# Performance work log

Hardware: AMD Instinct MI355X
Metric: run time of the kernel (lower is better)

## Reference

```python
import jax, jax.numpy as jnp
import numpy as np

B, D, H, G = 32768, 768, 256, 8
GS = D // G          # group size = 96
MIN_G, MAX_G = 2, 6  # min/max active groups


def setup_inputs() -> dict:
    key = jax.random.key(0)
    ks = jax.random.split(key, 12)
    s = 0.02
    return {
        "query_embedding": jax.random.normal(ks[0], (B, D), jnp.float32),
        # router_net: Linear(D,H) -> LayerNorm(H) -> GELU -> Linear(H,H//2) -> GELU -> Linear(H//2,G)
        "w1": jax.random.normal(ks[1], (D, H), jnp.float32) * s,
        "b1": jnp.zeros((H,), jnp.float32),
        "ln_g": jnp.ones((H,), jnp.float32),
        "ln_b": jnp.zeros((H,), jnp.float32),
        "w2": jax.random.normal(ks[2], (H, H // 2), jnp.float32) * s,
        "b2": jnp.zeros((H // 2,), jnp.float32),
        "w3": jax.random.normal(ks[3], (H // 2, G), jnp.float32) * s,
        "b3": jnp.zeros((G,), jnp.float32),
        # dim_importance: Linear(D,H) -> GELU -> Linear(H,D) (bias init 2.0) -> Sigmoid
        "dw1": jax.random.normal(ks[4], (D, H), jnp.float32) * s,
        "db1": jnp.zeros((H,), jnp.float32),
        "dw2": jax.random.normal(ks[5], (H, D), jnp.float32) * s,
        "db2": jnp.full((D,), 2.0, jnp.float32),
        "group_importance": jax.random.normal(ks[6], (G,), jnp.float32) * s,
    }


def _gelu(x):
    return jax.nn.gelu(x, approximate=False)  # torch nn.GELU default = exact erf


def _layernorm(x, g, b, eps=1e-5):
    mu = jnp.mean(x, axis=-1, keepdims=True)
    var = jnp.var(x, axis=-1, keepdims=True)
    return (x - mu) * jax.lax.rsqrt(var + eps) * g + b


def reference(query_embedding, w1, b1, ln_g, ln_b, w2, b2, w3, b3,
              dw1, db1, dw2, db2, group_importance):
    x = query_embedding
    # router_net (eval mode: dropout is identity, sigmoid gating not gumbel)
    h1 = _gelu(_layernorm(x @ w1 + b1, ln_g, ln_b))
    h2 = _gelu(h1 @ w2 + b2)
    group_logits = h2 @ w3 + b3 + group_importance          # [B, G]
    group_probs = jax.nn.sigmoid(group_logits)

    # constrained hard selection: top MIN_G always on; ranks MIN_G..MAX_G-1 on iff prob > 0.5
    order = jnp.argsort(-group_probs, axis=-1)              # descending sort indices [B, G]
    sorted_probs = jnp.take_along_axis(group_probs, order, axis=-1)
    ranks = jnp.arange(G)
    act_sorted = jnp.where(ranks < MIN_G, 1.0,
                           jnp.where(ranks < MAX_G,
                                     (sorted_probs > 0.5).astype(jnp.float32), 0.0))
    b_idx = jnp.arange(x.shape[0])[:, None]
    hard_mask = jnp.zeros_like(group_probs).at[b_idx, order].set(act_sorted)
    # straight-through estimator
    group_selection = hard_mask - jax.lax.stop_gradient(group_probs) + group_probs

    # expand each group decision over its group_size dims -> [B, D]
    group_mask = jnp.repeat(group_selection, GS, axis=-1)

    dim_weights = jax.nn.sigmoid(_gelu(x @ dw1 + db1) @ dw2 + db2)  # [B, D]
    mask = group_mask * dim_weights

    active_groups = jnp.mean(jnp.sum((group_probs > 0.5).astype(jnp.float32), axis=-1))
    group_usage = jnp.mean((group_probs > 0.5).astype(jnp.float32), axis=0)
    f = jnp.mean(group_probs, axis=0)
    load_balance = G * jnp.sum(f * (1.0 / G))
    active_dims = jnp.mean(jnp.sum((mask > 0.5).astype(jnp.float32), axis=-1))

    return (mask, group_mask, dim_weights, group_probs, group_selection,
            active_groups, group_usage, load_balance, active_dims)
```

## Files before the change

kernel.cpp:

```cpp
#include <hip/hip_runtime.h>
#include <math.h>

#define NB 32768
#define ND 768
#define NH 256
#define NG 8
#define GSZ 96

typedef __attribute__((ext_vector_type(8))) short short8_t;
typedef __attribute__((ext_vector_type(4))) float f32x4;

__device__ __forceinline__ float gelu_exact(float v) {
    return 0.5f * v * (1.0f + erff(v * 0.7071067811865475f));
}
__device__ __forceinline__ float sigmoidf_(float v) {
    return 1.0f / (1.0f + expf(-v));
}
__device__ __forceinline__ unsigned short f2bf(float f) {
    union { float f; unsigned u; } a; a.f = f;
    unsigned r = a.u + 0x7FFF + ((a.u >> 16) & 1);
    return (unsigned short)(r >> 16);
}
__device__ __forceinline__ void f2bf2(float f, unsigned short& hi, unsigned short& lo) {
    union { float f; unsigned u; } a; a.f = f;
    unsigned r = a.u + 0x7FFF + ((a.u >> 16) & 1);
    hi = (unsigned short)(r >> 16);
    union { unsigned u; float f; } hf; hf.u = (r >> 16) << 16;
    float rem = f - hf.f;
    union { float f; unsigned u; } b; b.f = rem;
    unsigned r2 = b.u + 0x7FFF + ((b.u >> 16) & 1);
    lo = (unsigned short)(r2 >> 16);
}

__global__ __launch_bounds__(256) void cvt_wall(
    const float* __restrict__ w1, const float* __restrict__ dw1,
    const float* __restrict__ dw2, const float* __restrict__ w2,
    unsigned short* __restrict__ w1Th, unsigned short* __restrict__ w1Tl,
    unsigned short* __restrict__ dw1T, unsigned short* __restrict__ dw2T,
    unsigned short* __restrict__ w2Th, unsigned short* __restrict__ w2Tl,
    float* __restrict__ scal)
{
    const int b = blockIdx.x, t = threadIdx.x;
    if (b < 96) {
        int idx = b * 256 + t;
        int k8 = idx >> 8, c = idx & 255;
        short8_t h, lo;
        #pragma unroll
        for (int j = 0; j < 8; ++j) {
            unsigned short hi_, lo_;
            f2bf2(w1[(size_t)(k8 * 8 + j) * 256 + c], hi_, lo_);
            h[j] = (short)hi_; lo[j] = (short)lo_;
        }
        *(short8_t*)(w1Th + (size_t)c * 768 + k8 * 8) = h;
        *(short8_t*)(w1Tl + (size_t)c * 768 + k8 * 8) = lo;
    } else if (b < 192) {
        int idx = (b - 96) * 256 + t;
        int k8 = idx >> 8, c = idx & 255;
        short8_t h;
        #pragma unroll
        for (int j = 0; j < 8; ++j)
            h[j] = (short)f2bf(dw1[(size_t)(k8 * 8 + j) * 256 + c]);
        *(short8_t*)(dw1T + (size_t)c * 768 + k8 * 8) = h;
    } else if (b < 288) {
        int idx = (b - 192) * 256 + t;
        int k8 = idx / 768, c = idx - k8 * 768;
        short8_t h;
        #pragma unroll
        for (int j = 0; j < 8; ++j)
            h[j] = (short)f2bf(dw2[(size_t)(k8 * 8 + j) * 768 + c]);
        *(short8_t*)(dw2T + (size_t)c * 256 + k8 * 8) = h;
    } else if (b < 304) {
        int idx = (b - 288) * 256 + t;
        int k8 = idx >> 7, c = idx & 127;
        short8_t h, lo;
        #pragma unroll
        for (int j = 0; j < 8; ++j) {
            unsigned short hi_, lo_;
            f2bf2(w2[(size_t)(k8 * 8 + j) * 128 + c], hi_, lo_);
            h[j] = (short)hi_; lo[j] = (short)lo_;
        }
        *(short8_t*)(w2Th + (size_t)c * 256 + k8 * 8) = h;
        *(short8_t*)(w2Tl + (size_t)c * 256 + k8 * 8) = lo;
    } else {
        if (t < 11) scal[t] = 0.0f;
    }
}

__global__ __launch_bounds__(256) void mfma_u1(
    const float* __restrict__ x, const unsigned short* __restrict__ BTh,
    const unsigned short* __restrict__ BTl, float* __restrict__ u1)
{
    __shared__ unsigned short Ah[128][40];
    __shared__ unsigned short Al[128][40];
    __shared__ unsigned short Bh[128][40];
    __shared__ unsigned short Bl[128][40];

    const int tid = threadIdx.x;
    const int l = tid & 63;
    const int w = tid >> 6;
    const int wm = w >> 1, wn = w & 1;
    const int lg = l >> 4, lr = l & 15;
    const int rb = blockIdx.x >> 1;
    const int cb = blockIdx.x & 1;
    const int rowsBase = rb * 128, colBase = cb * 128;

    f32x4 acc[4][4];
    #pragma unroll
    for (int mi = 0; mi < 4; ++mi)
        #pragma unroll
        for (int ni = 0; ni < 4; ++ni) acc[mi][ni] = (f32x4){0.f, 0.f, 0.f, 0.f};

    for (int kb = 0; kb < ND; kb += 32) {
        #pragma unroll
        for (int m = 0; m < 2; ++m) {
            int flat = m * 256 + tid;
            int row = flat >> 2, seg = flat & 3;
            const float* src = x + (size_t)(rowsBase + row) * ND + kb + seg * 8;
            float4 v0 = *(const float4*)src;
            float4 v1 = *(const float4*)(src + 4);
            float f[8] = {v0.x, v0.y, v0.z, v0.w, v1.x, v1.y, v1.z, v1.w};
            short8_t ph, pl;
            #pragma unroll
            for (int j = 0; j < 8; ++j) {
                unsigned short hi_, lo_;
                f2bf2(f[j], hi_, lo_);
                ph[j] = (short)hi_; pl[j] = (short)lo_;
            }
            *(short8_t*)&Ah[row][seg * 8] = ph;
            *(short8_t*)&Al[row][seg * 8] = pl;
        }
        #pragma unroll
        for (int m = 0; m < 2; ++m) {
            int flat = m * 256 + tid;
            int col = flat >> 2, seg = flat & 3;
            size_t off = (size_t)(colBase + col) * ND + kb + seg * 8;
            *(short8_t*)&Bh[col][seg * 8] = *(const short8_t*)(BTh + off);
            *(short8_t*)&Bl[col][seg * 8] = *(const short8_t*)(BTl + off);
        }
        __syncthreads();

        short8_t afh[4], afl[4], bfh[4], bfl[4];
        #pragma unroll
        for (int mi = 0; mi < 4; ++mi) {
            afh[mi] = *(const short8_t*)&Ah[wm * 64 + mi * 16 + lr][lg * 8];
            afl[mi] = *(const short8_t*)&Al[wm * 64 + mi * 16 + lr][lg * 8];
        }
        #pragma unroll
        for (int ni = 0; ni < 4; ++ni) {
            bfh[ni] = *(const short8_t*)&Bh[wn * 64 + ni * 16 + lr][lg * 8];
            bfl[ni] = *(const short8_t*)&Bl[wn * 64 + ni * 16 + lr][lg * 8];
        }
        #pragma unroll
        for (int mi = 0; mi < 4; ++mi)
            #pragma unroll
            for (int ni = 0; ni < 4; ++ni) {
                acc[mi][ni] = __builtin_amdgcn_mfma_f32_16x16x32_bf16(
                    afl[mi], bfh[ni], acc[mi][ni], 0, 0, 0);
                acc[mi][ni] = __builtin_amdgcn_mfma_f32_16x16x32_bf16(
                    afh[mi], bfl[ni], acc[mi][ni], 0, 0, 0);
                acc[mi][ni] = __builtin_amdgcn_mfma_f32_16x16x32_bf16(
                    afh[mi], bfh[ni], acc[mi][ni], 0, 0, 0);
            }
        __syncthreads();
    }

    #pragma unroll
    for (int ni = 0; ni < 4; ++ni) {
        int col = colBase + wn * 64 + ni * 16 + lr;
        #pragma unroll
        for (int mi = 0; mi < 4; ++mi) {
            int rbase = rowsBase + wm * 64 + mi * 16 + lg * 4;
            #pragma unroll
            for (int j = 0; j < 4; ++j)
                u1[(size_t)(rbase + j) * 256 + col] = acc[mi][ni][j];
        }
    }
}

__global__ __launch_bounds__(256) void k1_epi(
    const float* __restrict__ u1, const float* __restrict__ b1,
    const float* __restrict__ lng, const float* __restrict__ lnb,
    float* __restrict__ h1)
{
    const int wv = threadIdx.x >> 6, l = threadIdx.x & 63;
    const int row = blockIdx.x * 4 + wv;
    float4 a = *(const float4*)(u1 + (size_t)row * 256 + l * 4);
    float4 bb = *(const float4*)(b1 + l * 4);
    float u[4] = {a.x + bb.x, a.y + bb.y, a.z + bb.z, a.w + bb.w};
    float s = u[0] + u[1] + u[2] + u[3];
    float q = u[0]*u[0] + u[1]*u[1] + u[2]*u[2] + u[3]*u[3];
    #pragma unroll
    for (int o = 1; o < 64; o <<= 1) {
        s += __shfl_xor(s, o);
        q += __shfl_xor(q, o);
    }
    float mean = s * (1.0f / 256.0f);
    float var  = q * (1.0f / 256.0f) - mean * mean;
    float rstd = rsqrtf(var + 1e-5f);
    float4 g = *(const float4*)(lng + l * 4);
    float4 be = *(const float4*)(lnb + l * 4);
    float4 o;
    o.x = gelu_exact((u[0] - mean) * rstd * g.x + be.x);
    o.y = gelu_exact((u[1] - mean) * rstd * g.y + be.y);
    o.z = gelu_exact((u[2] - mean) * rstd * g.z + be.z);
    o.w = gelu_exact((u[3] - mean) * rstd * g.w + be.w);
    *(float4*)(h1 + (size_t)row * 256 + l * 4) = o;
}

__global__ __launch_bounds__(256) void mfma_u2(
    const float* __restrict__ h1, const unsigned short* __restrict__ BTh,
    const unsigned short* __restrict__ BTl, float* __restrict__ u2)
{
    __shared__ unsigned short Ah[128][40];
    __shared__ unsigned short Al[128][40];
    __shared__ unsigned short Bh[128][40];
    __shared__ unsigned short Bl[128][40];

    const int tid = threadIdx.x;
    const int l = tid & 63;
    const int w = tid >> 6;
    const int wm = w >> 1, wn = w & 1;
    const int lg = l >> 4, lr = l & 15;
    const int rowsBase = blockIdx.x * 128;

    f32x4 acc[4][4];
    #pragma unroll
    for (int mi = 0; mi < 4; ++mi)
        #pragma unroll
        for (int ni = 0; ni < 4; ++ni) acc[mi][ni] = (f32x4){0.f, 0.f, 0.f, 0.f};

    for (int kb = 0; kb < 256; kb += 32) {
        #pragma unroll
        for (int m = 0; m < 2; ++m) {
            int flat = m * 256 + tid;
            int row = flat >> 2, seg = flat & 3;
            const float* src = h1 + (size_t)(rowsBase + row) * 256 + kb + seg * 8;
            float4 v0 = *(const float4*)src;
            float4 v1 = *(const float4*)(src + 4);
            float f[8] = {v0.x, v0.y, v0.z, v0.w, v1.x, v1.y, v1.z, v1.w};
            short8_t ph, pl;
            #pragma unroll
            for (int j = 0; j < 8; ++j) {
                unsigned short hi_, lo_;
                f2bf2(f[j], hi_, lo_);
                ph[j] = (short)hi_; pl[j] = (short)lo_;
            }
            *(short8_t*)&Ah[row][seg * 8] = ph;
            *(short8_t*)&Al[row][seg * 8] = pl;
        }
        #pragma unroll
        for (int m = 0; m < 2; ++m) {
            int flat = m * 256 + tid;
            int col = flat >> 2, seg = flat & 3;
            size_t off = (size_t)col * 256 + kb + seg * 8;
            *(short8_t*)&Bh[col][seg * 8] = *(const short8_t*)(BTh + off);
            *(short8_t*)&Bl[col][seg * 8] = *(const short8_t*)(BTl + off);
        }
        __syncthreads();

        short8_t afh[4], afl[4], bfh[4], bfl[4];
        #pragma unroll
        for (int mi = 0; mi < 4; ++mi) {
            afh[mi] = *(const short8_t*)&Ah[wm * 64 + mi * 16 + lr][lg * 8];
            afl[mi] = *(const short8_t*)&Al[wm * 64 + mi * 16 + lr][lg * 8];
        }
        #pragma unroll
        for (int ni = 0; ni < 4; ++ni) {
            bfh[ni] = *(const short8_t*)&Bh[wn * 64 + ni * 16 + lr][lg * 8];
            bfl[ni] = *(const short8_t*)&Bl[wn * 64 + ni * 16 + lr][lg * 8];
        }
        #pragma unroll
        for (int mi = 0; mi < 4; ++mi)
            #pragma unroll
            for (int ni = 0; ni < 4; ++ni) {
                acc[mi][ni] = __builtin_amdgcn_mfma_f32_16x16x32_bf16(
                    afl[mi], bfh[ni], acc[mi][ni], 0, 0, 0);
                acc[mi][ni] = __builtin_amdgcn_mfma_f32_16x16x32_bf16(
                    afh[mi], bfl[ni], acc[mi][ni], 0, 0, 0);
                acc[mi][ni] = __builtin_amdgcn_mfma_f32_16x16x32_bf16(
                    afh[mi], bfh[ni], acc[mi][ni], 0, 0, 0);
            }
        __syncthreads();
    }

    #pragma unroll
    for (int ni = 0; ni < 4; ++ni) {
        int col = wn * 64 + ni * 16 + lr;
        #pragma unroll
        for (int mi = 0; mi < 4; ++mi) {
            int rbase = rowsBase + wm * 64 + mi * 16 + lg * 4;
            #pragma unroll
            for (int j = 0; j < 4; ++j)
                u2[(size_t)(rbase + j) * 128 + col] = acc[mi][ni][j];
        }
    }
}

template<int ACT, int AF32>
__global__ __launch_bounds__(256) void mfma_hi(
    const void* __restrict__ Ap, const unsigned short* __restrict__ BT,
    const float* __restrict__ bias, void* __restrict__ outp,
    int N, int K, int colBlocks)
{
    __shared__ unsigned short As[128][40];
    __shared__ unsigned short Bs[128][40];

    const int tid = threadIdx.x;
    const int l = tid & 63;
    const int w = tid >> 6;
    const int wm = w >> 1, wn = w & 1;
    const int lg = l >> 4, lr = l & 15;
    const int rb = blockIdx.x / colBlocks;
    const int cb = blockIdx.x - rb * colBlocks;
    const int rowsBase = rb * 128, colBase = cb * 128;

    f32x4 acc[4][4];
    #pragma unroll
    for (int mi = 0; mi < 4; ++mi)
        #pragma unroll
        for (int ni = 0; ni < 4; ++ni) acc[mi][ni] = (f32x4){0.f, 0.f, 0.f, 0.f};

    for (int kb = 0; kb < K; kb += 32) {
        if (AF32) {
            const float* A = (const float*)Ap;
            #pragma unroll
            for (int m = 0; m < 2; ++m) {
                int flat = m * 256 + tid;
                int row = flat >> 2, seg = flat & 3;
                const float* src = A + (size_t)(rowsBase + row) * K + kb + seg * 8;
                float4 v0 = *(const float4*)src;
                float4 v1 = *(const float4*)(src + 4);
                float f[8] = {v0.x, v0.y, v0.z, v0.w, v1.x, v1.y, v1.z, v1.w};
                short8_t h;
                #pragma unroll
                for (int j = 0; j < 8; ++j) h[j] = (short)f2bf(f[j]);
                *(short8_t*)&As[row][seg * 8] = h;
            }
        } else {
            const unsigned short* A = (const unsigned short*)Ap;
            #pragma unroll
            for (int m = 0; m < 2; ++m) {
                int flat = m * 256 + tid;
                int row = flat >> 2, seg = flat & 3;
                *(short8_t*)&As[row][seg * 8] =
                    *(const short8_t*)(A + (size_t)(rowsBase + row) * K + kb + seg * 8);
            }
        }
        #pragma unroll
        for (int m = 0; m < 2; ++m) {
            int flat = m * 256 + tid;
            int col = flat >> 2, seg = flat & 3;
            *(short8_t*)&Bs[col][seg * 8] =
                *(const short8_t*)(BT + (size_t)(colBase + col) * K + kb + seg * 8);
        }
        __syncthreads();

        short8_t af[4], bf[4];
        #pragma unroll
        for (int mi = 0; mi < 4; ++mi)
            af[mi] = *(const short8_t*)&As[wm * 64 + mi * 16 + lr][lg * 8];
        #pragma unroll
        for (int ni = 0; ni < 4; ++ni)
            bf[ni] = *(const short8_t*)&Bs[wn * 64 + ni * 16 + lr][lg * 8];
        #pragma unroll
        for (int mi = 0; mi < 4; ++mi)
            #pragma unroll
            for (int ni = 0; ni < 4; ++ni)
                acc[mi][ni] = __builtin_amdgcn_mfma_f32_16x16x32_bf16(
                    af[mi], bf[ni], acc[mi][ni], 0, 0, 0);
        __syncthreads();
    }

    #pragma unroll
    for (int ni = 0; ni < 4; ++ni) {
        int col = colBase + wn * 64 + ni * 16 + lr;
        float bv = bias[col];
        #pragma unroll
        for (int mi = 0; mi < 4; ++mi) {
            int rbase = rowsBase + wm * 64 + mi * 16 + lg * 4;
            #pragma unroll
            for (int j = 0; j < 4; ++j) {
                float v = acc[mi][ni][j] + bv;
                if (ACT == 0) {
                    ((unsigned short*)outp)[(size_t)(rbase + j) * N + col] =
                        f2bf(gelu_exact(v));
                } else {
                    ((float*)outp)[(size_t)(rbase + j) * N + col] = sigmoidf_(v);
                }
            }
        }
    }
}

__global__ __launch_bounds__(128) void k3_router(
    const float* __restrict__ u2, const float* __restrict__ w3,
    const float* __restrict__ b3, const float* __restrict__ gi,
    const float* __restrict__ b2, float* __restrict__ probsOut,
    float* __restrict__ selOut, float* __restrict__ scal)
{
    __shared__ float ws3[128][8];
    __shared__ float sAct[2], sP[2], sCnt[2][8];

    const int tid = threadIdx.x;
    *(float4*)&ws3[tid][0] = *(const float4*)(w3 + tid * 8);
    *(float4*)&ws3[tid][4] = *(const float4*)(w3 + tid * 8 + 4);
    __syncthreads();

    const int row = blockIdx.x * 128 + tid;
    const float* r0p = u2 + (size_t)row * 128;

    float accg[8];
    #pragma unroll
    for (int g = 0; g < 8; ++g) accg[g] = 0.0f;
    #pragma unroll 4
    for (int k4 = 0; k4 < 32; ++k4) {
        float4 a = *(const float4*)(r0p + k4 * 4);
        float4 bb = *(const float4*)(b2 + k4 * 4);
        float hv4[4];
        hv4[0] = gelu_exact(a.x + bb.x);
        hv4[1] = gelu_exact(a.y + bb.y);
        hv4[2] = gelu_exact(a.z + bb.z);
        hv4[3] = gelu_exact(a.w + bb.w);
        #pragma unroll
        for (int t = 0; t < 4; ++t)
            #pragma unroll
            for (int g = 0; g < 8; ++g)
                accg[g] = fmaf(hv4[t], ws3[k4 * 4 + t][g], accg[g]);
    }

    float p[8], gs[8], cnt[8];
    float actCnt = 0.0f, pSum = 0.0f;
    #pragma unroll
    for (int g = 0; g < 8; ++g) {
        float lg = accg[g] + b3[g] + gi[g];
        p[g] = sigmoidf_(lg);
    }
    #pragma unroll
    for (int g = 0; g < 8; ++g) {
        int rank = 0;
        #pragma unroll
        for (int j = 0; j < 8; ++j) {
            rank += (p[j] > p[g]) ? 1 : 0;
            rank += (j < g && p[j] == p[g]) ? 1 : 0;
        }
        float act = (rank < 2) ? 1.0f
                  : ((rank < 6) ? ((p[g] > 0.5f) ? 1.0f : 0.0f) : 0.0f);
        gs[g] = (act - p[g]) + p[g];
        float over = (p[g] > 0.5f) ? 1.0f : 0.0f;
        cnt[g] = over;
        actCnt += over;
        pSum += p[g];
    }

    *(float4*)(probsOut + (size_t)row * 8)     = *(float4*)&p[0];
    *(float4*)(probsOut + (size_t)row * 8 + 4) = *(float4*)&p[4];
    *(float4*)(selOut   + (size_t)row * 8)     = *(float4*)&gs[0];
    *(float4*)(selOut   + (size_t)row * 8 + 4) = *(float4*)&gs[4];

    #pragma unroll
    for (int o = 32; o > 0; o >>= 1) {
        actCnt += __shfl_down(actCnt, o);
        pSum   += __shfl_down(pSum, o);
        #pragma unroll
        for (int g = 0; g < 8; ++g) cnt[g] += __shfl_down(cnt[g], o);
    }
    if ((tid & 63) == 0) {
        int w = tid >> 6;
        sAct[w] = actCnt; sP[w] = pSum;
        #pragma unroll
        for (int g = 0; g < 8; ++g) sCnt[w][g] = cnt[g];
    }
    __syncthreads();
    if (tid == 0) {
        const float invB = 1.0f / 32768.0f;
        atomicAdd(&scal[0], (sAct[0] + sAct[1]) * invB);
        atomicAdd(&scal[9], (sP[0] + sP[1]) * invB);
        #pragma unroll
        for (int g = 0; g < 8; ++g)
            atomicAdd(&scal[1 + g], (sCnt[0][g] + sCnt[1][g]) * invB);
    }
}

__global__ __launch_bounds__(256) void k4_mask(
    const float* __restrict__ sel, const float* __restrict__ dwts,
    float* __restrict__ gmaskOut, float* __restrict__ maskOut,
    float* __restrict__ activeDims)
{
    const int stride = gridDim.x * 256;
    float cntF = 0.0f;
    for (int i4 = blockIdx.x * 256 + threadIdx.x; i4 < 6291456; i4 += stride) {
        int row = i4 / 192;
        int rem = i4 - row * 192;
        int g = rem / 24;
        float v = sel[(size_t)row * 8 + g];
        float4 d = *(const float4*)(dwts + (size_t)i4 * 4);
        float4 gm = {v, v, v, v};
        float4 m = {v * d.x, v * d.y, v * d.z, v * d.w};
        *(float4*)(gmaskOut + (size_t)i4 * 4) = gm;
        *(float4*)(maskOut  + (size_t)i4 * 4) = m;
        cntF += (m.x > 0.5f ? 1.0f : 0.0f) + (m.y > 0.5f ? 1.0f : 0.0f)
              + (m.z > 0.5f ? 1.0f : 0.0f) + (m.w > 0.5f ? 1.0f : 0.0f);
    }
    #pragma unroll
    for (int o = 32; o > 0; o >>= 1) cntF += __shfl_down(cntF, o);
    __shared__ float sc[4];
    if ((threadIdx.x & 63) == 0) sc[threadIdx.x >> 6] = cntF;
    __syncthreads();
    if (threadIdx.x == 0)
        atomicAdd(activeDims, (sc[0] + sc[1] + sc[2] + sc[3]) * (1.0f / 32768.0f));
}

extern "C" void kernel_launch(void* const* d_in, const int* in_sizes, int n_in,
                              void* d_out, int out_size, void* d_ws, size_t ws_size,
                              hipStream_t stream)
{
    const float* x   = (const float*)d_in[0];
    const float* w1  = (const float*)d_in[1];
    const float* b1  = (const float*)d_in[2];
    const float* lng = (const float*)d_in[3];
    const float* lnb = (const float*)d_in[4];
    const float* w2  = (const float*)d_in[5];
    const float* b2  = (const float*)d_in[6];
    const float* w3  = (const float*)d_in[7];
    const float* b3  = (const float*)d_in[8];
    const float* dw1 = (const float*)d_in[9];
    const float* db1 = (const float*)d_in[10];
    const float* dw2 = (const float*)d_in[11];
    const float* db2 = (const float*)d_in[12];
    const float* gi  = (const float*)d_in[13];

    float* out   = (float*)d_out;
    float* mask  = out;
    float* gmask = out + 25165824;
    float* dwts  = out + 50331648;
    float* probs = out + 75497472;
    float* sel   = out + 75759616;
    float* scal  = out + 76021760;

    float* u1 = mask;
    float* h1 = mask + 8388608;
    float* u2 = mask + 16777216;
    unsigned short* g1h  = (unsigned short*)gmask;
    unsigned short* w1Th = (unsigned short*)(gmask + 4194304);
    unsigned short* w1Tl = (unsigned short*)(gmask + 4292608);
    unsigned short* dw1T = (unsigned short*)(gmask + 4390912);
    unsigned short* dw2T = (unsigned short*)(gmask + 4489216);
    unsigned short* w2Th = (unsigned short*)(gmask + 4587520);
    unsigned short* w2Tl = (unsigned short*)(gmask + 4603904);

    cvt_wall<<<dim3(305), dim3(256), 0, stream>>>(
        w1, dw1, dw2, w2, w1Th, w1Tl, dw1T, dw2T, w2Th, w2Tl, scal);
    mfma_u1<<<dim3(512), dim3(256), 0, stream>>>(x, w1Th, w1Tl, u1);
    k1_epi<<<dim3(8192), dim3(256), 0, stream>>>(u1, b1, lng, lnb, h1);
    mfma_u2<<<dim3(256), dim3(256), 0, stream>>>(h1, w2Th, w2Tl, u2);
    k3_router<<<dim3(256), dim3(128), 0, stream>>>(
        u2, w3, b3, gi, b2, probs, sel, scal);
    mfma_hi<0, 1><<<dim3(512), dim3(256), 0, stream>>>(
        (const void*)x, dw1T, db1, (void*)g1h, 256, 768, 2);
    mfma_hi<1, 0><<<dim3(1536), dim3(256), 0, stream>>>(
        (const void*)g1h, dw2T, db2, (void*)dwts, 768, 256, 6);
    k4_mask<<<dim3(2048), dim3(256), 0, stream>>>(sel, dwts, gmask, mask, &scal[10]);
}
```

Measured before the change: 284.0 us.

## Fuse dim-importance GEMMs with router GEMM launch and mask epilogue

Merges the router first-layer split-bf16 GEMM and the dim_importance first-layer GEMM into one 512-thread kernel, with block role chosen by block index. Both use 128x256 tiles. The second dim_importance GEMM now computes sigmoid, the mask product and the active-dims count in its epilogue. That removes the separate pass that re-read the full dim_weights array, leaving a lighter kernel that only writes group_mask. The cost is larger tiles with more LDS per block, branches on block role, and strided scalar stores in the epilogue.

```diff
diff --git a/kernel.cpp b/kernel.cpp
--- a/kernel.cpp
+++ b/kernel.cpp
@@ -86,23 +86,24 @@
     }
 }
 
-__global__ __launch_bounds__(256) void mfma_u1(
-    const float* __restrict__ x, const unsigned short* __restrict__ BTh,
-    const unsigned short* __restrict__ BTl, float* __restrict__ u1)
+__global__ __launch_bounds__(512) void mfma_pair(
+    const float* __restrict__ x,
+    const unsigned short* __restrict__ w1Th, const unsigned short* __restrict__ w1Tl,
+    const unsigned short* __restrict__ dw1T, const float* __restrict__ db1,
+    float* __restrict__ u1, unsigned short* __restrict__ g1h)
 {
     __shared__ unsigned short Ah[128][40];
     __shared__ unsigned short Al[128][40];
-    __shared__ unsigned short Bh[128][40];
-    __shared__ unsigned short Bl[128][40];
+    __shared__ unsigned short Bh[256][40];
+    __shared__ unsigned short Bl[256][40];
 
     const int tid = threadIdx.x;
     const int l = tid & 63;
     const int w = tid >> 6;
-    const int wm = w >> 1, wn = w & 1;
+    const int wm = w >> 2, wn = w & 3;
     const int lg = l >> 4, lr = l & 15;
-    const int rb = blockIdx.x >> 1;
-    const int cb = blockIdx.x & 1;
-    const int rowsBase = rb * 128, colBase = cb * 128;
+    const bool splitRole = blockIdx.x < 256;
+    const int rowsBase = (blockIdx.x & 255) * 128;
 
     f32x4 acc[4][4];
     #pragma unroll
@@ -110,69 +111,107 @@
         #pragma unroll
         for (int ni = 0; ni < 4; ++ni) acc[mi][ni] = (f32x4){0.f, 0.f, 0.f, 0.f};
 
+    const int sArow = tid >> 2, sAseg = tid & 3;
+
     for (int kb = 0; kb < ND; kb += 32) {
-        #pragma unroll
-        for (int m = 0; m < 2; ++m) {
-            int flat = m * 256 + tid;
-            int row = flat >> 2, seg = flat & 3;
-            const float* src = x + (size_t)(rowsBase + row) * ND + kb + seg * 8;
+        {
+            const float* src = x + (size_t)(rowsBase + sArow) * ND + kb + sAseg * 8;
             float4 v0 = *(const float4*)src;
             float4 v1 = *(const float4*)(src + 4);
             float f[8] = {v0.x, v0.y, v0.z, v0.w, v1.x, v1.y, v1.z, v1.w};
-            short8_t ph, pl;
-            #pragma unroll
-            for (int j = 0; j < 8; ++j) {
-                unsigned short hi_, lo_;
-                f2bf2(f[j], hi_, lo_);
-                ph[j] = (short)hi_; pl[j] = (short)lo_;
-            }
-            *(short8_t*)&Ah[row][seg * 8] = ph;
-            *(short8_t*)&Al[row][seg * 8] = pl;
+            if (splitRole) {
+                short8_t ph, pl;
+                #pragma unroll
+                for (int j = 0; j < 8; ++j) {
+                    unsigned short hi_, lo_;
+                    f2bf2(f[j], hi_, lo_);
+                    ph[j] = (short)hi_; pl[j] = (short)lo_;
+                }
+                *(short8_t*)&Ah[sArow][sAseg * 8] = ph;
+                *(short8_t*)&Al[sArow][sAseg * 8] = pl;
+            } else {
+                short8_t ph;
+                #pragma unroll
+                for (int j = 0; j < 8; ++j) ph[j] = (short)f2bf(f[j]);
+                *(short8_t*)&Ah[sArow][sAseg * 8] = ph;
+            }
         }
         #pragma unroll
         for (int m = 0; m < 2; ++m) {
-            int flat = m * 256 + tid;
+            int flat = m * 512 + tid;
             int col = flat >> 2, seg = flat & 3;
-            size_t off = (size_t)(colBase + col) * ND + kb + seg * 8;
-            *(short8_t*)&Bh[col][seg * 8] = *(const short8_t*)(BTh + off);
-            *(short8_t*)&Bl[col][seg * 8] = *(const short8_t*)(BTl + off);
+            size_t off = (size_t)col * ND + kb + seg * 8;
+            if (splitRole) {
+                *(short8_t*)&Bh[col][seg * 8] = *(const short8_t*)(w1Th + off);
+                *(short8_t*)&Bl[col][seg * 8] = *(const short8_t*)(w1Tl + off);
+            } else {
+                *(short8_t*)&Bh[col][seg * 8] = *(const short8_t*)(dw1T + off);
+            }
         }
         __syncthreads();
 
-        short8_t afh[4], afl[4], bfh[4], bfl[4];
-        #pragma unroll
-        for (int mi = 0; mi < 4; ++mi) {
+        short8_t afh[4], bfh[4];
+        #pragma unroll
+        for (int mi = 0; mi < 4; ++mi)
             afh[mi] = *(const short8_t*)&Ah[wm * 64 + mi * 16 + lr][lg * 8];
-            afl[mi] = *(const short8_t*)&Al[wm * 64 + mi * 16 + lr][lg * 8];
-        }
+        #pragma unroll
+        for (int ni = 0; ni < 4; ++ni)
+            bfh[ni] = *(const short8_t*)&Bh[wn * 64 + ni * 16 + lr][lg * 8];
+        if (splitRole) {
+            short8_t afl[4], bfl[4];
+            #pragma unroll
+            for (int mi = 0; mi < 4; ++mi)
+                afl[mi] = *(const short8_t*)&Al[wm * 64 + mi * 16 + lr][lg * 8];
+            #pragma unroll
+            for (int ni = 0; ni < 4; ++ni)
+                bfl[ni] = *(const short8_t*)&Bl[wn * 64 + ni * 16 + lr][lg * 8];
+            #pragma unroll
+            for (int mi = 0; mi < 4; ++mi)
+                #pragma unroll
+                for (int ni = 0; ni < 4; ++ni) {
+                    acc[mi][ni] = __builtin_amdgcn_mfma_f32_16x16x32_bf16(
+                        afl[mi], bfh[ni], acc[mi][ni], 0, 0, 0);
+                    acc[mi][ni] = __builtin_amdgcn_mfma_f32_16x16x32_bf16(
+                        afh[mi], bfl[ni], acc[mi][ni], 0, 0, 0);
+                    acc[mi][ni] = __builtin_amdgcn_mfma_f32_16x16x32_bf16(
+                        afh[mi], bfh[ni], acc[mi][ni], 0, 0, 0);
+                }
+        } else {
+            #pragma unroll
+            for (int mi = 0; mi < 4; ++mi)
+                #pragma unroll
+                for (int ni = 0; ni < 4; ++ni)
+                    acc[mi][ni] = __builtin_amdgcn_mfma_f32_16x16x32_bf16(
+                        afh[mi], bfh[ni], acc[mi][ni], 0, 0, 0);
+        }
+        __syncthreads();
+    }
+
+    if (splitRole) {
         #pragma unroll
         for (int ni = 0; ni < 4; ++ni) {
-            bfh[ni] = *(const short8_t*)&Bh[wn * 64 + ni * 16 + lr][lg * 8];
-            bfl[ni] = *(const short8_t*)&Bl[wn * 64 + ni * 16 + lr][lg * 8];
-        }
-        #pragma unroll
-        for (int mi = 0; mi < 4; ++mi)
-            #pragma unroll
-            for (int ni = 0; ni < 4; ++ni) {
-                acc[mi][ni] = __builtin_amdgcn_mfma_f32_16x16x32_bf16(
-                    afl[mi], bfh[ni], acc[mi][ni], 0, 0, 0);
-                acc[mi][ni] = __builtin_amdgcn_mfma_f32_16x16x32_bf16(
-                    afh[mi], bfl[ni], acc[mi][ni], 0, 0, 0);
-                acc[mi][ni] = __builtin_amdgcn_mfma_f32_16x16x32_bf16(
-                    afh[mi], bfh[ni], acc[mi][ni], 0, 0, 0);
-            }
-        __syncthreads();
-    }
-
-    #pragma unroll
-    for (int ni = 0; ni < 4; ++ni) {
-        int col = colBase + wn * 64 + ni * 16 + lr;
-        #pragma unroll
-        for (int mi = 0; mi < 4; ++mi) {
-            int rbase = rowsBase + wm * 64 + mi * 16 + lg * 4;
-            #pragma unroll
-            for (int j = 0; j < 4; ++j)
-                u1[(size_t)(rbase + j) * 256 + col] = acc[mi][ni][j];
+            int col = wn * 64 + ni * 16 + lr;
+            #pragma unroll
+            for (int mi = 0; mi < 4; ++mi) {
+                int rbase = rowsBase + wm * 64 + mi * 16 + lg * 4;
+                #pragma unroll
+                for (int j = 0; j < 4; ++j)
+                    u1[(size_t)(rbase + j) * 256 + col] = acc[mi][ni][j];
+            }
+        }
+    } else {
+        #pragma unroll
+        for (int ni = 0; ni < 4; ++ni) {
+            int col = wn * 64 + ni * 16 + lr;
+            float bv = db1[col];
+            #pragma unroll
+            for (int mi = 0; mi < 4; ++mi) {
+                int rbase = rowsBase + wm * 64 + mi * 16 + lg * 4;
+                #pragma unroll
+                for (int j = 0; j < 4; ++j)
+                    g1h[(size_t)(rbase + j) * 256 + col] =
+                        f2bf(gelu_exact(acc[mi][ni][j] + bv));
+            }
         }
     }
 }
@@ -296,102 +335,6 @@
     }
 }
 
-template<int ACT, int AF32>
-__global__ __launch_bounds__(256) void mfma_hi(
-    const void* __restrict__ Ap, const unsigned short* __restrict__ BT,
-    const float* __restrict__ bias, void* __restrict__ outp,
-    int N, int K, int colBlocks)
-{
-    __shared__ unsigned short As[128][40];
-    __shared__ unsigned short Bs[128][40];
-
-    const int tid = threadIdx.x;
-    const int l = tid & 63;
-    const int w = tid >> 6;
-    const int wm = w >> 1, wn = w & 1;
-    const int lg = l >> 4, lr = l & 15;
-    const int rb = blockIdx.x / colBlocks;
-    const int cb = blockIdx.x - rb * colBlocks;
-    const int rowsBase = rb * 128, colBase = cb * 128;
-
-    f32x4 acc[4][4];
-    #pragma unroll
-    for (int mi = 0; mi < 4; ++mi)
-        #pragma unroll
-        for (int ni = 0; ni < 4; ++ni) acc[mi][ni] = (f32x4){0.f, 0.f, 0.f, 0.f};
-
-    for (int kb = 0; kb < K; kb += 32) {
-        if (AF32) {
-            const float* A = (const float*)Ap;
-            #pragma unroll
-            for (int m = 0; m < 2; ++m) {
-                int flat = m * 256 + tid;
-                int row = flat >> 2, seg = flat & 3;
-                const float* src = A + (size_t)(rowsBase + row) * K + kb + seg * 8;
-                float4 v0 = *(const float4*)src;
-                float4 v1 = *(const float4*)(src + 4);
-                float f[8] = {v0.x, v0.y, v0.z, v0.w, v1.x, v1.y, v1.z, v1.w};
-                short8_t h;
-                #pragma unroll
-                for (int j = 0; j < 8; ++j) h[j] = (short)f2bf(f[j]);
-                *(short8_t*)&As[row][seg * 8] = h;
-            }
-        } else {
-            const unsigned short* A = (const unsigned short*)Ap;
-            #pragma unroll
-            for (int m = 0; m < 2; ++m) {
-                int flat = m * 256 + tid;
-                int row = flat >> 2, seg = flat & 3;
-                *(short8_t*)&As[row][seg * 8] =
-                    *(const short8_t*)(A + (size_t)(rowsBase + row) * K + kb + seg * 8);
-            }
-        }
-        #pragma unroll
-        for (int m = 0; m < 2; ++m) {
-            int flat = m * 256 + tid;
-            int col = flat >> 2, seg = flat & 3;
-            *(short8_t*)&Bs[col][seg * 8] =
-                *(const short8_t*)(BT + (size_t)(colBase + col) * K + kb + seg * 8);
-        }
-        __syncthreads();
-
-        short8_t af[4], bf[4];
-        #pragma unroll
-        for (int mi = 0; mi < 4; ++mi)
-            af[mi] = *(const short8_t*)&As[wm * 64 + mi * 16 + lr][lg * 8];
-        #pragma unroll
-        for (int ni = 0; ni < 4; ++ni)
-            bf[ni] = *(const short8_t*)&Bs[wn * 64 + ni * 16 + lr][lg * 8];
-        #pragma unroll
-        for (int mi = 0; mi < 4; ++mi)
-            #pragma unroll
-            for (int ni = 0; ni < 4; ++ni)
-                acc[mi][ni] = __builtin_amdgcn_mfma_f32_16x16x32_bf16(
-                    af[mi], bf[ni], acc[mi][ni], 0, 0, 0);
-        __syncthreads();
-    }
-
-    #pragma unroll
-    for (int ni = 0; ni < 4; ++ni) {
-        int col = colBase + wn * 64 + ni * 16 + lr;
-        float bv = bias[col];
-        #pragma unroll
-        for (int mi = 0; mi < 4; ++mi) {
-            int rbase = rowsBase + wm * 64 + mi * 16 + lg * 4;
-            #pragma unroll
-            for (int j = 0; j < 4; ++j) {
-                float v = acc[mi][ni][j] + bv;
-                if (ACT == 0) {
-                    ((unsigned short*)outp)[(size_t)(rbase + j) * N + col] =
-                        f2bf(gelu_exact(v));
-                } else {
-                    ((float*)outp)[(size_t)(rbase + j) * N + col] = sigmoidf_(v);
-                }
-            }
-        }
-    }
-}
-
 __global__ __launch_bounds__(128) void k3_router(
     const float* __restrict__ u2, const float* __restrict__ w3,
     const float* __restrict__ b3, const float* __restrict__ gi,
@@ -481,33 +424,101 @@
     }
 }
 
-__global__ __launch_bounds__(256) void k4_mask(
-    const float* __restrict__ sel, const float* __restrict__ dwts,
-    float* __restrict__ gmaskOut, float* __restrict__ maskOut,
+__global__ __launch_bounds__(512) void mfma_dw2m(
+    const unsigned short* __restrict__ g1h, const unsigned short* __restrict__ dw2T,
+    const float* __restrict__ db2, const float* __restrict__ sel,
+    float* __restrict__ dwts, float* __restrict__ maskOut,
     float* __restrict__ activeDims)
 {
+    __shared__ unsigned short As[128][40];
+    __shared__ unsigned short Bs[256][40];
+    __shared__ float sc[8];
+
+    const int tid = threadIdx.x;
+    const int l = tid & 63;
+    const int w = tid >> 6;
+    const int wm = w >> 2, wn = w & 3;
+    const int lg = l >> 4, lr = l & 15;
+    const int rb = blockIdx.x / 3, cb = blockIdx.x - rb * 3;
+    const int rowsBase = rb * 128, colBase = cb * 256;
+
+    f32x4 acc[4][4];
+    #pragma unroll
+    for (int mi = 0; mi < 4; ++mi)
+        #pragma unroll
+        for (int ni = 0; ni < 4; ++ni) acc[mi][ni] = (f32x4){0.f, 0.f, 0.f, 0.f};
+
+    const int sArow = tid >> 2, sAseg = tid & 3;
+
+    for (int kb = 0; kb < 256; kb += 32) {
+        *(short8_t*)&As[sArow][sAseg * 8] =
+            *(const short8_t*)(g1h + (size_t)(rowsBase + sArow) * 256 + kb + sAseg * 8);
+        #pragma unroll
+        for (int m = 0; m < 2; ++m) {
+            int flat = m * 512 + tid;
+            int col = flat >> 2, seg = flat & 3;
+            *(short8_t*)&Bs[col][seg * 8] =
+                *(const short8_t*)(dw2T + (size_t)(colBase + col) * 256 + kb + seg * 8);
+        }
+        __syncthreads();
+
+        short8_t af[4], bf[4];
+        #pragma unroll
+        for (int mi = 0; mi < 4; ++mi)
+            af[mi] = *(const short8_t*)&As[wm * 64 + mi * 16 + lr][lg * 8];
+        #pragma unroll
+        for (int ni = 0; ni < 4; ++ni)
+            bf[ni] = *(const short8_t*)&Bs[wn * 64 + ni * 16 + lr][lg * 8];
+        #pragma unroll
+        for (int mi = 0; mi < 4; ++mi)
+            #pragma unroll
+            for (int ni = 0; ni < 4; ++ni)
+                acc[mi][ni] = __builtin_amdgcn_mfma_f32_16x16x32_bf16(
+                    af[mi], bf[ni], acc[mi][ni], 0, 0, 0);
+        __syncthreads();
+    }
+
+    float cntF = 0.0f;
+    #pragma unroll
+    for (int ni = 0; ni < 4; ++ni) {
+        int col = colBase + wn * 64 + ni * 16 + lr;
+        float bv = db2[col];
+        int g = col / GSZ;
+        #pragma unroll
+        for (int mi = 0; mi < 4; ++mi) {
+            int rbase = rowsBase + wm * 64 + mi * 16 + lg * 4;
+            #pragma unroll
+            for (int j = 0; j < 4; ++j) {
+                int row = rbase + j;
+                float v = sigmoidf_(acc[mi][ni][j] + bv);
+                dwts[(size_t)row * 768 + col] = v;
+                float m = sel[(size_t)row * 8 + g] * v;
+                maskOut[(size_t)row * 768 + col] = m;
+                cntF += (m > 0.5f) ? 1.0f : 0.0f;
+            }
+        }
+    }
+    #pragma unroll
+    for (int o = 32; o > 0; o >>= 1) cntF += __shfl_down(cntF, o);
+    if ((tid & 63) == 0) sc[tid >> 6] = cntF;
+    __syncthreads();
+    if (tid == 0)
+        atomicAdd(activeDims, (sc[0] + sc[1] + sc[2] + sc[3] +
+                               sc[4] + sc[5] + sc[6] + sc[7]) * (1.0f / 32768.0f));
+}
+
+__global__ __launch_bounds__(256) void k4_gmask(
+    const float* __restrict__ sel, float* __restrict__ gmaskOut)
+{
     const int stride = gridDim.x * 256;
-    float cntF = 0.0f;
     for (int i4 = blockIdx.x * 256 + threadIdx.x; i4 < 6291456; i4 += stride) {
         int row = i4 / 192;
         int rem = i4 - row * 192;
         int g = rem / 24;
         float v = sel[(size_t)row * 8 + g];
-        float4 d = *(const float4*)(dwts + (size_t)i4 * 4);
         float4 gm = {v, v, v, v};
-        float4 m = {v * d.x, v * d.y, v * d.z, v * d.w};
         *(float4*)(gmaskOut + (size_t)i4 * 4) = gm;
-        *(float4*)(maskOut  + (size_t)i4 * 4) = m;
-        cntF += (m.x > 0.5f ? 1.0f : 0.0f) + (m.y > 0.5f ? 1.0f : 0.0f)
-              + (m.z > 0.5f ? 1.0f : 0.0f) + (m.w > 0.5f ? 1.0f : 0.0f);
-    }
-    #pragma unroll
-    for (int o = 32; o > 0; o >>= 1) cntF += __shfl_down(cntF, o);
-    __shared__ float sc[4];
-    if ((threadIdx.x & 63) == 0) sc[threadIdx.x >> 6] = cntF;
-    __syncthreads();
-    if (threadIdx.x == 0)
-        atomicAdd(activeDims, (sc[0] + sc[1] + sc[2] + sc[3]) * (1.0f / 32768.0f));
+    }
 }
 
 extern "C" void kernel_launch(void* const* d_in, const int* in_sizes, int n_in,
@@ -550,14 +561,13 @@
 
     cvt_wall<<<dim3(305), dim3(256), 0, stream>>>(
         w1, dw1, dw2, w2, w1Th, w1Tl, dw1T, dw2T, w2Th, w2Tl, scal);
-    mfma_u1<<<dim3(512), dim3(256), 0, stream>>>(x, w1Th, w1Tl, u1);
+    mfma_pair<<<dim3(512), dim3(512), 0, stream>>>(
+        x, w1Th, w1Tl, dw1T, db1, u1, g1h);
     k1_epi<<<dim3(8192), dim3(256), 0, stream>>>(u1, b1, lng, lnb, h1);
     mfma_u2<<<dim3(256), dim3(256), 0, stream>>>(h1, w2Th, w2Tl, u2);
     k3_router<<<dim3(256), dim3(128), 0, stream>>>(
         u2, w3, b3, gi, b2, probs, sel, scal);
-    mfma_hi<0, 1><<<dim3(512), dim3(256), 0, stream>>>(
-        (const void*)x, dw1T, db1, (void*)g1h, 256, 768, 2);
-    mfma_hi<1, 0><<<dim3(1536), dim3(256), 0, stream>>>(
-        (const void*)g1h, dw2T, db2, (void*)dwts, 768, 256, 6);
-    k4_mask<<<dim3(2048), dim3(256), 0, stream>>>(sel, dwts, gmask, mask, &scal[10]);
-}
+    mfma_dw2m<<<dim3(768), dim3(512), 0, stream>>>(
+        g1h, dw2T, db2, sel, dwts, mask, &scal[10]);
+    k4_gmask<<<dim3(2048), dim3(256), 0, stream>>>(sel, gmask);
+}
```

Measured after the change: 290.1 us. 1.02x slower.

## Fuse dim_importance second GEMM with sigmoid, mask multiply and active-dims count

Applied to the files above, without the earlier changes.

Replaces the generic second dim_importance GEMM plus the separate mask kernel with one MFMA kernel. Its epilogue applies the sigmoid, writes dim_weights, multiplies by the group selection to write the mask, and accumulates the active-dims count. This removes a full re-read of dim_weights and one pass over the data, and a slimmed kernel now only writes group_mask. The first dim GEMM launch also moves earlier in the stream. The risk is that the epilogue's per-element stores have a 768-float row stride across lanes and coalesce less well than the previous float4 streaming writes.

```diff
diff --git a/kernel.cpp b/kernel.cpp
--- a/kernel.cpp
+++ b/kernel.cpp
@@ -481,33 +481,101 @@
     }
 }
 
-__global__ __launch_bounds__(256) void k4_mask(
-    const float* __restrict__ sel, const float* __restrict__ dwts,
-    float* __restrict__ gmaskOut, float* __restrict__ maskOut,
+__global__ __launch_bounds__(512) void mfma_dw2m(
+    const unsigned short* __restrict__ g1h, const unsigned short* __restrict__ dw2T,
+    const float* __restrict__ db2, const float* __restrict__ sel,
+    float* __restrict__ dwts, float* __restrict__ maskOut,
     float* __restrict__ activeDims)
 {
+    __shared__ unsigned short As[128][40];
+    __shared__ unsigned short Bs[256][40];
+    __shared__ float sc[8];
+
+    const int tid = threadIdx.x;
+    const int l = tid & 63;
+    const int w = tid >> 6;
+    const int wm = w >> 2, wn = w & 3;
+    const int lg = l >> 4, lr = l & 15;
+    const int rb = blockIdx.x / 3, cb = blockIdx.x - rb * 3;
+    const int rowsBase = rb * 128, colBase = cb * 256;
+
+    f32x4 acc[4][4];
+    #pragma unroll
+    for (int mi = 0; mi < 4; ++mi)
+        #pragma unroll
+        for (int ni = 0; ni < 4; ++ni) acc[mi][ni] = (f32x4){0.f, 0.f, 0.f, 0.f};
+
+    const int sArow = tid >> 2, sAseg = tid & 3;
+
+    for (int kb = 0; kb < 256; kb += 32) {
+        *(short8_t*)&As[sArow][sAseg * 8] =
+            *(const short8_t*)(g1h + (size_t)(rowsBase + sArow) * 256 + kb + sAseg * 8);
+        #pragma unroll
+        for (int m = 0; m < 2; ++m) {
+            int flat = m * 512 + tid;
+            int col = flat >> 2, seg = flat & 3;
+            *(short8_t*)&Bs[col][seg * 8] =
+                *(const short8_t*)(dw2T + (size_t)(colBase + col) * 256 + kb + seg * 8);
+        }
+        __syncthreads();
+
+        short8_t af[4], bf[4];
+        #pragma unroll
+        for (int mi = 0; mi < 4; ++mi)
+            af[mi] = *(const short8_t*)&As[wm * 64 + mi * 16 + lr][lg * 8];
+        #pragma unroll
+        for (int ni = 0; ni < 4; ++ni)
+            bf[ni] = *(const short8_t*)&Bs[wn * 64 + ni * 16 + lr][lg * 8];
+        #pragma unroll
+        for (int mi = 0; mi < 4; ++mi)
+            #pragma unroll
+            for (int ni = 0; ni < 4; ++ni)
+                acc[mi][ni] = __builtin_amdgcn_mfma_f32_16x16x32_bf16(
+                    af[mi], bf[ni], acc[mi][ni], 0, 0, 0);
+        __syncthreads();
+    }
+
+    float cntF = 0.0f;
+    #pragma unroll
+    for (int ni = 0; ni < 4; ++ni) {
+        int col = colBase + wn * 64 + ni * 16 + lr;
+        float bv = db2[col];
+        int g = col / GSZ;
+        #pragma unroll
+        for (int mi = 0; mi < 4; ++mi) {
+            int rbase = rowsBase + wm * 64 + mi * 16 + lg * 4;
+            #pragma unroll
+            for (int j = 0; j < 4; ++j) {
+                int row = rbase + j;
+                float v = sigmoidf_(acc[mi][ni][j] + bv);
+                dwts[(size_t)row * 768 + col] = v;
+                float m = sel[(size_t)row * 8 + g] * v;
+                maskOut[(size_t)row * 768 + col] = m;
+                cntF += (m > 0.5f) ? 1.0f : 0.0f;
+            }
+        }
+    }
+    #pragma unroll
+    for (int o = 32; o > 0; o >>= 1) cntF += __shfl_down(cntF, o);
+    if ((tid & 63) == 0) sc[tid >> 6] = cntF;
+    __syncthreads();
+    if (tid == 0)
+        atomicAdd(activeDims, (sc[0] + sc[1] + sc[2] + sc[3] +
+                               sc[4] + sc[5] + sc[6] + sc[7]) * (1.0f / 32768.0f));
+}
+
+__global__ __launch_bounds__(256) void k4_gmask(
+    const float* __restrict__ sel, float* __restrict__ gmaskOut)
+{
     const int stride = gridDim.x * 256;
-    float cntF = 0.0f;
     for (int i4 = blockIdx.x * 256 + threadIdx.x; i4 < 6291456; i4 += stride) {
         int row = i4 / 192;
         int rem = i4 - row * 192;
         int g = rem / 24;
         float v = sel[(size_t)row * 8 + g];
-        float4 d = *(const float4*)(dwts + (size_t)i4 * 4);
         float4 gm = {v, v, v, v};
-        float4 m = {v * d.x, v * d.y, v * d.z, v * d.w};
         *(float4*)(gmaskOut + (size_t)i4 * 4) = gm;
-        *(float4*)(maskOut  + (size_t)i4 * 4) = m;
-        cntF += (m.x > 0.5f ? 1.0f : 0.0f) + (m.y > 0.5f ? 1.0f : 0.0f)
-              + (m.z > 0.5f ? 1.0f : 0.0f) + (m.w > 0.5f ? 1.0f : 0.0f);
-    }
-    #pragma unroll
-    for (int o = 32; o > 0; o >>= 1) cntF += __shfl_down(cntF, o);
-    __shared__ float sc[4];
-    if ((threadIdx.x & 63) == 0) sc[threadIdx.x >> 6] = cntF;
-    __syncthreads();
-    if (threadIdx.x == 0)
-        atomicAdd(activeDims, (sc[0] + sc[1] + sc[2] + sc[3]) * (1.0f / 32768.0f));
+    }
 }
 
 extern "C" void kernel_launch(void* const* d_in, const int* in_sizes, int n_in,
@@ -551,13 +619,13 @@
     cvt_wall<<<dim3(305), dim3(256), 0, stream>>>(
         w1, dw1, dw2, w2, w1Th, w1Tl, dw1T, dw2T, w2Th, w2Tl, scal);
     mfma_u1<<<dim3(512), dim3(256), 0, stream>>>(x, w1Th, w1Tl, u1);
+    mfma_hi<0, 1><<<dim3(512), dim3(256), 0, stream>>>(
+        (const void*)x, dw1T, db1, (void*)g1h, 256, 768, 2);
     k1_epi<<<dim3(8192), dim3(256), 0, stream>>>(u1, b1, lng, lnb, h1);
     mfma_u2<<<dim3(256), dim3(256), 0, stream>>>(h1, w2Th, w2Tl, u2);
     k3_router<<<dim3(256), dim3(128), 0, stream>>>(
         u2, w3, b3, gi, b2, probs, sel, scal);
-    mfma_hi<0, 1><<<dim3(512), dim3(256), 0, stream>>>(
-        (const void*)x, dw1T, db1, (void*)g1h, 256, 768, 2);
-    mfma_hi<1, 0><<<dim3(1536), dim3(256), 0, stream>>>(
-        (const void*)g1h, dw2T, db2, (void*)dwts, 768, 256, 6);
-    k4_mask<<<dim3(2048), dim3(256), 0, stream>>>(sel, dwts, gmask, mask, &scal[10]);
-}
+    mfma_dw2m<<<dim3(768), dim3(512), 0, stream>>>(
+        g1h, dw2T, db2, sel, dwts, mask, &scal[10]);
+    k4_gmask<<<dim3(2048), dim3(256), 0, stream>>>(sel, gmask);
+}
```

New measurement: 276.0 us, median of 2. -2.8%, faster.
